# Kernel optimization log

Hardware: AMD Instinct MI355X
Metric: run time of the kernel (lower is better)

## Reference

```python
import jax, jax.numpy as jnp
import numpy as np
from jax import lax

B, T, S = 32, 64, 400
H, E, EMB, V = 512, 1024, 256, 32000


def setup_inputs() -> dict:
    key = jax.random.key(0)
    ks = jax.random.split(key, 16)
    w = lambda k, shape: jax.random.normal(k, shape, dtype=jnp.float32) * 0.05
    return {
        "target": jax.random.randint(ks[0], (B, T), 0, V),
        "h0": jax.random.normal(ks[1], (B, H), dtype=jnp.float32),
        "c0": jax.random.normal(ks[2], (B, H), dtype=jnp.float32),
        "enc_outs": jax.random.normal(ks[3], (S, B, E), dtype=jnp.float32),
        "attn_mask": jnp.ones((B, S), dtype=jnp.int32),
        "emb": w(ks[4], (V, EMB)),
        "W_ih": w(ks[5], (4 * H, EMB)),
        "b_ih": w(ks[6], (4 * H,)),
        "W_hh": w(ks[7], (4 * H, H)),
        "b_hh": w(ks[8], (4 * H,)),
        "W_attn": w(ks[9], (H, E)),
        "b_attn": w(ks[10], (H,)),
        "W_concat": w(ks[11], (H, E + H)),
        "b_concat": w(ks[12], (H,)),
        "W_out": w(ks[13], (V, H)),
        "b_out": w(ks[14], (V,)),
    }


def reference(target, h0, c0, enc_outs, attn_mask, emb, W_ih, b_ih, W_hh, b_hh,
              W_attn, b_attn, W_concat, b_concat, W_out, b_out):
    # Precompute attention keys projection once: [S, B, H]
    keys_proj = jnp.einsum("sbe,he->sbh", enc_outs, W_attn) + b_attn
    masked = attn_mask == 0  # [B, S]
    x_seq = emb[target].transpose(1, 0, 2)  # [T, B, EMB]

    def step(carry, x_t):
        h, c = carry
        # LSTMCell (torch gate order: i, f, g, o)
        gates = x_t @ W_ih.T + b_ih + h @ W_hh.T + b_hh  # [B, 4H]
        i, f, g, o = jnp.split(gates, 4, axis=1)
        c = jax.nn.sigmoid(f) * c + jax.nn.sigmoid(i) * jnp.tanh(g)
        h = jax.nn.sigmoid(o) * jnp.tanh(c)
        # additive-style attention: sum over hidden of query*key_proj
        scores = jnp.einsum("bh,sbh->bs", h, keys_proj)  # [B, S]
        scores = jnp.where(masked, jnp.float32(-1e18), scores)
        a = jax.nn.softmax(scores, axis=1)
        ctx = jnp.einsum("bs,sbe->be", a, enc_outs)  # [B, E]
        cat = jnp.tanh(jnp.concatenate([ctx, h], axis=1) @ W_concat.T + b_concat)
        logit = jax.nn.log_softmax(cat @ W_out.T + b_out, axis=-1)  # [B, V]
        return (h, c), logit

    (_, _), logits = lax.scan(step, (h0, c0), x_seq)  # [T, B, V]
    return logits.transpose(1, 0, 2)  # [B, T, V]
```

## Files before the change

kernel.cpp:

```cpp
#include <hip/hip_runtime.h>
#include <hip/hip_bf16.h>
#include <hip/hip_fp16.h>

#define B_ 32
#define T_ 64
#define S_ 400
#define SPAD_ 512
#define H_ 512
#define E_ 1024
#define EMB_ 256
#define V_ 32000
#define NCB_ 500

#define KEYS_BLOCKS 200
#define CVT_BLOCKS 48
#define MEGA_BLOCKS (8 + KEYS_BLOCKS + CVT_BLOCKS)
#define MEGA_LDS (65536 + 33280 + 4096 + 32)

typedef _Float16 f16;
typedef _Float16 half8 __attribute__((ext_vector_type(8)));
typedef float f32x4 __attribute__((ext_vector_type(4)));
typedef float f32x16 __attribute__((ext_vector_type(16)));
typedef unsigned uint4v __attribute__((ext_vector_type(4)));

__device__ __forceinline__ void gl_lds16(const void* g, void* l) {
  __builtin_amdgcn_global_load_lds(
      (const __attribute__((address_space(1))) void*)g,
      (__attribute__((address_space(3))) void*)l, 16, 0, 0);
}

__device__ __forceinline__ float sigmoidf_(float x) { return 1.f / (1.f + expf(-x)); }

__device__ __forceinline__ uint4v load_b128_sys(const void* p) {
  uint4v r;
  asm volatile("global_load_dwordx4 %0, %1, off sc0 sc1" : "=v"(r) : "v"(p) : "memory");
  return r;
}
__device__ __forceinline__ void store_b128_sys(void* p, uint4v v) {
  asm volatile("global_store_dwordx4 %0, %1, off sc0 sc1" :: "v"(p), "v"(v) : "memory");
}

__global__ __launch_bounds__(256) void gather_x_kernel(const int* __restrict__ target,
                                                       const float* __restrict__ emb,
                                                       f16* __restrict__ xin) {
  int r = blockIdx.x;
  int t = r >> 5, b = r & 31;
  int tok = target[b * T_ + t];
  xin[(size_t)r * EMB_ + threadIdx.x] = (f16)emb[(size_t)tok * EMB_ + threadIdx.x];
}

__global__ __launch_bounds__(256) void prep_kernel(const float* __restrict__ b_ih,
                                                   const float* __restrict__ b_hh,
                                                   float* __restrict__ biasperm,
                                                   const float* __restrict__ Whh,
                                                   f16* __restrict__ Wperm,
                                                   const float* __restrict__ Wih,
                                                   f16* __restrict__ Wihp,
                                                   const float* __restrict__ h0,
                                                   f16* __restrict__ hbuf,
                                                   const float* __restrict__ Wattn,
                                                   f16* __restrict__ Wattn_f) {
  int idx = blockIdx.x * 256 + threadIdx.x;
  if (idx < 4 * H_) {
    int j = idx >> 2, gg = idx & 3;
    biasperm[idx] = b_ih[gg * H_ + j] + b_hh[gg * H_ + j];
  }
  if (idx < B_ * H_) hbuf[idx] = (f16)h0[idx];
  if (idx < T_ * B_ * H_ / 8) {
    uint4v p = {0xFFFFFFFFu, 0xFFFFFFFFu, 0xFFFFFFFFu, 0xFFFFFFFFu};
    reinterpret_cast<uint4v*>(reinterpret_cast<char*>(hbuf) + (size_t)B_ * H_ * 2)[idx] = p;
  }
  {
    int j = idx >> 9, k = idx & 511;
#pragma unroll
    for (int gg = 0; gg < 4; ++gg)
      Wperm[((size_t)(j * 4 + gg)) * H_ + k] = (f16)Whh[((size_t)(gg * H_ + j)) * H_ + k];
  }
  if (idx < H_ * EMB_) {
    int j = idx >> 8, k = idx & 255;
#pragma unroll
    for (int gg = 0; gg < 4; ++gg)
      Wihp[((size_t)(j * 4 + gg)) * EMB_ + k] = (f16)Wih[((size_t)(gg * H_ + j)) * EMB_ + k];
  }
  {
    float2 v = reinterpret_cast<const float2*>(Wattn)[idx];
    union { f16 h[2]; unsigned u; } o;
    o.h[0] = (f16)v.x; o.h[1] = (f16)v.y;
    reinterpret_cast<unsigned*>(Wattn_f)[idx] = o.u;
  }
}

template <int OUTK, bool DO_TANH>
__global__ __launch_bounds__(256) void gemm_bt_kernel(const f16* __restrict__ A,
                                                      const f16* __restrict__ W,
                                                      const float* __restrict__ bias,
                                                      void* __restrict__ outp,
                                                      int M, int N, int K) {
  __shared__ __align__(16) char As[128 * 64];
  __shared__ __align__(16) char Bs[128 * 64];
  const int tid = threadIdx.x;
  const int lane = tid & 63, wave = tid >> 6;
  const int wr = (wave >> 1) * 64, wc = (wave & 1) * 64;
  const int fr = lane & 15, fq = lane >> 4;
  const int row0 = blockIdx.x * 128, col0 = blockIdx.y * 128;

  f32x4 acc[4][4];
#pragma unroll
  for (int i = 0; i < 4; ++i)
#pragma unroll
    for (int j = 0; j < 4; ++j) acc[i][j] = {0.f, 0.f, 0.f, 0.f};

  for (int k0 = 0; k0 < K; k0 += 32) {
    __syncthreads();
#pragma unroll
    for (int i = 0; i < 2; ++i) {
      int o = tid * 16 + i * 4096;
      int r = o >> 6, kk = (o & 63) >> 1;
      gl_lds16(A + (size_t)(row0 + r) * K + (k0 + kk), As + o);
      gl_lds16(W + (size_t)(col0 + r) * K + (k0 + kk), Bs + o);
    }
    __syncthreads();
    half8 af[4], bfr[4];
#pragma unroll
    for (int mi = 0; mi < 4; ++mi)
      af[mi] = *reinterpret_cast<const half8*>(As + (wr + mi * 16 + fr) * 64 + fq * 16);
#pragma unroll
    for (int ni = 0; ni < 4; ++ni)
      bfr[ni] = *reinterpret_cast<const half8*>(Bs + (wc + ni * 16 + fr) * 64 + fq * 16);
#pragma unroll
    for (int mi = 0; mi < 4; ++mi)
#pragma unroll
      for (int ni = 0; ni < 4; ++ni)
        acc[mi][ni] = __builtin_amdgcn_mfma_f32_16x16x32_f16(af[mi], bfr[ni], acc[mi][ni], 0, 0, 0);
  }

#pragma unroll
  for (int mi = 0; mi < 4; ++mi)
#pragma unroll
    for (int ni = 0; ni < 4; ++ni)
#pragma unroll
      for (int r = 0; r < 4; ++r) {
        int row = row0 + wr + mi * 16 + fq * 4 + r;
        int col = col0 + wc + ni * 16 + fr;
        float v = acc[mi][ni][r] + bias[col];
        if (DO_TANH) v = tanhf(v);
        if (OUTK == 0) {
          ((float*)outp)[(size_t)row * N + col] = v;
        } else if (OUTK == 1) {
          ((f16*)outp)[(size_t)row * N + col] = (f16)v;
        } else {
          int orow = (row & 31) * T_ + (row >> 5);
          ((float*)outp)[(size_t)orow * N + col] = v;
        }
      }
}

__global__ __launch_bounds__(512, 1) void mega_kernel(
    const float* __restrict__ xpart, const f16* __restrict__ Wperm,
    const float* __restrict__ c0, f16* __restrict__ hbuf,
    const float* __restrict__ enc, const f16* __restrict__ Wattn_f,
    const float* __restrict__ b_attn, f16* __restrict__ keys,
    const float* __restrict__ wc_src, f16* __restrict__ wc_dst,
    const float* __restrict__ wo_src, f16* __restrict__ wo_dst) {
  extern __shared__ char lds[];
  const int blk = blockIdx.x, tid = threadIdx.x;
  const int lane = tid & 63, wave = tid >> 6;

  if (blk < 8) {
    char* Abuf = lds;
    float* gates = (float*)(lds + 65536);
    unsigned* hstage = (unsigned*)(lds + 65536 + 33280);
    int* flags = (int*)(lds + 65536 + 33280 + 4096);
    const int g = blk;
    const int ln31 = lane & 31, lh = lane >> 5;

    if (tid < 8) flags[tid] = 0;

    half8 wf[32];
    {
      const f16* wrow = Wperm + ((size_t)(g * 256 + wave * 32 + ln31)) * H_ + lh * 8;
#pragma unroll
      for (int kc = 0; kc < 32; ++kc)
        wf[kc] = *reinterpret_cast<const half8*>(wrow + kc * 16);
    }

    const int b = tid >> 4, qd = tid & 15;
    float cst[4];
#pragma unroll
    for (int jj = 0; jj < 4; ++jj)
      cst[jj] = c0[b * H_ + g * 64 + qd * 4 + jj];

    __syncthreads();

    for (int t = 0; t < T_; ++t) {
      const float* xr = xpart + ((size_t)(t * B_ + b)) * (4 * H_) + g * 256 + qd * 16;
      float4 xv[4];
#pragma unroll
      for (int i = 0; i < 4; ++i) xv[i] = *reinterpret_cast<const float4*>(xr + i * 4);

      {
        int p = (t == 0) ? wave : (wave + (wave >= g ? 1 : 0));
        bool duty = (t == 0) ? true : (wave < 7);
        if (duty) {
          const char* sb = (const char*)hbuf + (size_t)t * 32768 + ln31 * 1024 + p * 128 + lh * 16;
          while (true) {
            uint4v v0 = load_b128_sys(sb);
            uint4v v1 = load_b128_sys(sb + 32);
            uint4v v2 = load_b128_sys(sb + 64);
            uint4v v3 = load_b128_sys(sb + 96);
            asm volatile("s_waitcnt vmcnt(0)" ::: "memory");
            __builtin_amdgcn_sched_barrier(0);
            unsigned bad = 0;
#pragma unroll
            for (int d = 0; d < 4; ++d)
              bad |= (unsigned)(v0[d] == 0xFFFFFFFFu) | (unsigned)(v1[d] == 0xFFFFFFFFu) |
                     (unsigned)(v2[d] == 0xFFFFFFFFu) | (unsigned)(v3[d] == 0xFFFFFFFFu);
            if (__all(bad == 0)) {
              char* ab = Abuf + (size_t)(t & 1) * 32768 + lane * 16;
              *(uint4v*)(ab + (size_t)(4 * p + 0) * 1024) = v0;
              *(uint4v*)(ab + (size_t)(4 * p + 1) * 1024) = v1;
              *(uint4v*)(ab + (size_t)(4 * p + 2) * 1024) = v2;
              *(uint4v*)(ab + (size_t)(4 * p + 3) * 1024) = v3;
              asm volatile("s_waitcnt lgkmcnt(0)" ::: "memory");
              __builtin_amdgcn_sched_barrier(0);
              if (lane == 0)
                __hip_atomic_fetch_add(&flags[p], 1, __ATOMIC_RELAXED,
                                       __HIP_MEMORY_SCOPE_WORKGROUP);
              break;
            }
          }
        }
      }

      f32x16 acc;
#pragma unroll
      for (int r = 0; r < 16; ++r) acc[r] = 0.f;
      const char* abR = Abuf + (size_t)(t & 1) * 32768 + lane * 16;
      const char* hsR = (const char*)hstage + lane * 16;
      const int thr = t + 1;
#pragma unroll
      for (int ps = 0; ps < 8; ++ps) {
        if (ps == g && t > 0) {
#pragma unroll
          for (int c = 0; c < 4; ++c) {
            half8 a = *(const half8*)(hsR + c * 1024);
            acc = __builtin_amdgcn_mfma_f32_32x32x16_f16(a, wf[4 * ps + c], acc, 0, 0, 0);
          }
        } else {
          while (__hip_atomic_load(&flags[ps], __ATOMIC_ACQUIRE,
                                   __HIP_MEMORY_SCOPE_WORKGROUP) < thr) {}
#pragma unroll
          for (int c = 0; c < 4; ++c) {
            half8 a = *(const half8*)(abR + (size_t)(4 * ps + c) * 1024);
            acc = __builtin_amdgcn_mfma_f32_32x32x16_f16(a, wf[4 * ps + c], acc, 0, 0, 0);
          }
        }
      }
      const int ln31b = lane & 31, lhb = lane >> 5;
#pragma unroll
      for (int r = 0; r < 16; ++r) {
        int row = (r & 3) + 8 * (r >> 2) + 4 * lhb;
        gates[row * 260 + wave * 32 + ln31b] = acc[r];
      }
      __syncthreads();

      const float* gr = &gates[b * 260 + qd * 16];
      float hv[4];
#pragma unroll
      for (int jj = 0; jj < 4; ++jj) {
        float gi = gr[jj * 4 + 0] + xv[jj].x;
        float gf = gr[jj * 4 + 1] + xv[jj].y;
        float gg = gr[jj * 4 + 2] + xv[jj].z;
        float go = gr[jj * 4 + 3] + xv[jj].w;
        cst[jj] = sigmoidf_(gf) * cst[jj] + sigmoidf_(gi) * tanhf(gg);
        hv[jj] = sigmoidf_(go) * tanhf(cst[jj]);
      }
      union { f16 h[2]; unsigned u; } pk0, pk1;
      pk0.h[0] = (f16)hv[0]; pk0.h[1] = (f16)hv[1];
      pk1.h[0] = (f16)hv[2]; pk1.h[1] = (f16)hv[3];
      {
        int cp0 = 2 * qd, cp1 = 2 * qd + 1;
        hstage[((cp0 >> 3) * 64 + ((cp0 >> 2) & 1) * 32 + b) * 4 + (cp0 & 3)] = pk0.u;
        hstage[((cp1 >> 3) * 64 + ((cp1 >> 2) & 1) * 32 + b) * 4 + (cp1 & 3)] = pk1.u;
      }
      __syncthreads();

      if (tid < 256) {
        int kcl = tid >> 6, l2 = tid & 63;
        uint4v v = *(const uint4v*)((const char*)hstage + (kcl * 64 + l2) * 16);
        store_b128_sys((char*)hbuf + (size_t)(t + 1) * 32768 + (l2 & 31) * 1024 +
                           g * 128 + kcl * 32 + (l2 >> 5) * 16,
                       v);
      }
    }
  } else if (blk < 8 + KEYS_BLOCKS) {
    char* As = lds;
    char* Bs = lds + 16384;
    const int kid = blk - 8;
    const int row0 = (kid % 50) * 256, col0 = (kid / 50) * 128;
    const int wr = (wave >> 1) * 64, wc = (wave & 1) * 64;
    const int fr = lane & 15, fq = lane >> 4;

    f32x4 acc[4][4];
#pragma unroll
    for (int i = 0; i < 4; ++i)
#pragma unroll
      for (int j = 0; j < 4; ++j) acc[i][j] = {0.f, 0.f, 0.f, 0.f};

    for (int k0 = 0; k0 < E_; k0 += 32) {
      __syncthreads();
      float4 av[4];
#pragma unroll
      for (int i = 0; i < 4; ++i) {
        int idx = tid + i * 512;
        int r = idx >> 3, ck = (idx & 7) * 4;
        av[i] = *reinterpret_cast<const float4*>(enc + (size_t)(row0 + r) * E_ + k0 + ck);
      }
      {
        int o = tid * 16;
        int r = o >> 6, kk = (o & 63) >> 1;
        gl_lds16(Wattn_f + (size_t)(col0 + r) * E_ + (k0 + kk), Bs + o);
      }
#pragma unroll
      for (int i = 0; i < 4; ++i) {
        int idx = tid + i * 512;
        int r = idx >> 3, ck = (idx & 7) * 4;
        union { f16 h[4]; unsigned long long u; } p;
        p.h[0] = (f16)av[i].x; p.h[1] = (f16)av[i].y;
        p.h[2] = (f16)av[i].z; p.h[3] = (f16)av[i].w;
        *reinterpret_cast<unsigned long long*>(As + r * 64 + ck * 2) = p.u;
      }
      __syncthreads();
      half8 af[4], bf[4];
#pragma unroll
      for (int mi = 0; mi < 4; ++mi)
        af[mi] = *reinterpret_cast<const half8*>(As + (wr + mi * 16 + fr) * 64 + fq * 16);
#pragma unroll
      for (int ni = 0; ni < 4; ++ni)
        bf[ni] = *reinterpret_cast<const half8*>(Bs + (wc + ni * 16 + fr) * 64 + fq * 16);
#pragma unroll
      for (int mi = 0; mi < 4; ++mi)
#pragma unroll
        for (int ni = 0; ni < 4; ++ni)
          acc[mi][ni] = __builtin_amdgcn_mfma_f32_16x16x32_f16(af[mi], bf[ni], acc[mi][ni], 0, 0, 0);
    }
#pragma unroll
    for (int mi = 0; mi < 4; ++mi)
#pragma unroll
      for (int ni = 0; ni < 4; ++ni)
#pragma unroll
        for (int r = 0; r < 4; ++r) {
          int row = row0 + wr + mi * 16 + fq * 4 + r;
          int col = col0 + wc + ni * 16 + fr;
          keys[(size_t)row * H_ + col] = (f16)(acc[mi][ni][r] + b_attn[col]);
        }
  } else {
    const int N2WC = H_ * (E_ + H_) / 2, N2WO = V_ * H_ / 2;
    const int total = N2WC + N2WO;
    const int stride = CVT_BLOCKS * 512;
    for (int i = (blk - 8 - KEYS_BLOCKS) * 512 + tid; i < total; i += stride) {
      const float* s; f16* d; int j;
      if (i < N2WC) { s = wc_src; d = wc_dst; j = i; }
      else { s = wo_src; d = wo_dst; j = i - N2WC; }
      float2 v = reinterpret_cast<const float2*>(s)[j];
      union { f16 h[2]; unsigned u; } o;
      o.h[0] = (f16)v.x; o.h[1] = (f16)v.y;
      reinterpret_cast<unsigned*>(d)[j] = o.u;
    }
  }
}

__global__ __launch_bounds__(128) void catcopy_kernel(const f16* __restrict__ hseq,
                                                      f16* __restrict__ catin) {
  int r = blockIdx.x;
  const uint2* src = reinterpret_cast<const uint2*>(hseq + (size_t)r * H_);
  uint2* dst = reinterpret_cast<uint2*>(catin + (size_t)r * (E_ + H_) + E_);
  dst[threadIdx.x] = src[threadIdx.x];
}

__global__ __launch_bounds__(256) void scores_mfma_kernel(const f16* __restrict__ keys,
                                                          const f16* __restrict__ hseq,
                                                          float* __restrict__ attnw) {
  const int b = blockIdx.y;
  const int lane = threadIdx.x & 63, wave = threadIdx.x >> 6;
  const int ln31 = lane & 31, lh = lane >> 5;
  const int stile = blockIdx.x * 128 + wave * 32;
  const f16* ar  = keys + ((size_t)(stile + ln31) * B_ + b) * H_ + lh * 8;
  const f16* br0 = hseq + ((size_t)ln31 * B_ + b) * H_ + lh * 8;
  const f16* br1 = hseq + ((size_t)(ln31 + 32) * B_ + b) * H_ + lh * 8;
  f32x16 ac0, ac1;
#pragma unroll
  for (int r = 0; r < 16; ++r) { ac0[r] = 0.f; ac1[r] = 0.f; }
#pragma unroll
  for (int kc = 0; kc < 32; ++kc) {
    half8 a  = *reinterpret_cast<const half8*>(ar + kc * 16);
    half8 h0 = *reinterpret_cast<const half8*>(br0 + kc * 16);
    half8 h1 = *reinterpret_cast<const half8*>(br1 + kc * 16);
    ac0 = __builtin_amdgcn_mfma_f32_32x32x16_f16(a, h0, ac0, 0, 0, 0);
    ac1 = __builtin_amdgcn_mfma_f32_32x32x16_f16(a, h1, ac1, 0, 0, 0);
  }
#pragma unroll
  for (int r = 0; r < 16; ++r) {
    int s = stile + (r & 3) + 8 * (r >> 2) + 4 * lh;
    if (s < S_) {
      attnw[((size_t)b * S_ + s) * T_ + ln31]      = ac0[r];
      attnw[((size_t)b * S_ + s) * T_ + 32 + ln31] = ac1[r];
    }
  }
}

__global__ __launch_bounds__(64) void softmax_kernel(float* __restrict__ attnw,
                                                     const int* __restrict__ mask) {
  int b = blockIdx.x, t = blockIdx.y, l = threadIdx.x;
  float vals[7];
  float m = -3.4e38f;
#pragma unroll
  for (int i = 0; i < 7; ++i) {
    int s = l + i * 64;
    float v = -3.4e38f;
    if (s < S_) {
      v = attnw[((size_t)b * S_ + s) * T_ + t];
      if (mask[b * S_ + s] == 0) v = -1e18f;
    }
    vals[i] = v;
    m = fmaxf(m, v);
  }
#pragma unroll
  for (int o = 32; o > 0; o >>= 1) m = fmaxf(m, __shfl_xor(m, o));
  float sum = 0.f;
#pragma unroll
  for (int i = 0; i < 7; ++i) {
    int s = l + i * 64;
    if (s < S_) { float e = expf(vals[i] - m); vals[i] = e; sum += e; }
  }
#pragma unroll
  for (int o = 32; o > 0; o >>= 1) sum += __shfl_xor(sum, o);
  float inv = 1.f / sum;
#pragma unroll
  for (int i = 0; i < 7; ++i) {
    int s = l + i * 64;
    if (s < S_) attnw[((size_t)b * S_ + s) * T_ + t] = vals[i] * inv;
  }
}

__global__ __launch_bounds__(256) void ctx_kernel(const float* __restrict__ attnw,
                                                  const float* __restrict__ enc,
                                                  f16* __restrict__ catin) {
  int b = blockIdx.x, e0 = blockIdx.y * 64;
  int el = threadIdx.x & 63, tq = threadIdx.x >> 6;
  __shared__ float a_lds[100 * 64];
  float acc[16];
#pragma unroll
  for (int i = 0; i < 16; ++i) acc[i] = 0.f;
  for (int sc = 0; sc < 4; ++sc) {
    __syncthreads();
    for (int i = threadIdx.x; i < 6400; i += 256)
      a_lds[i] = attnw[((size_t)b * S_ + sc * 100) * T_ + i];
    __syncthreads();
    for (int sl = 0; sl < 100; ++sl) {
      int s = sc * 100 + sl;
      float v = enc[((size_t)s * B_ + b) * E_ + e0 + el];
#pragma unroll
      for (int i = 0; i < 16; ++i) acc[i] += a_lds[sl * 64 + tq * 16 + i] * v;
    }
  }
#pragma unroll
  for (int i = 0; i < 16; ++i) {
    int t = tq * 16 + i;
    catin[((size_t)t * B_ + b) * (E_ + H_) + e0 + el] = (f16)acc[i];
  }
}

__global__ __launch_bounds__(256) void gemm_out_kernel(const f16* __restrict__ A,
                                                       const f16* __restrict__ W,
                                                       const float* __restrict__ bias,
                                                       f16* __restrict__ lbuf,
                                                       float* __restrict__ pm,
                                                       float* __restrict__ ps) {
  __shared__ __align__(16) char As[128 * 64];
  __shared__ __align__(16) char Bs[128 * 64];
  const int tid = threadIdx.x;
  const int lane = tid & 63, wave = tid >> 6;
  const int wr = (wave >> 1) * 64, wc = (wave & 1) * 64;
  const int fr = lane & 15, fq = lane >> 4;
  const int row0 = blockIdx.x * 128, col0 = blockIdx.y * 128;

  f32x4 acc[4][4];
#pragma unroll
  for (int i = 0; i < 4; ++i)
#pragma unroll
    for (int j = 0; j < 4; ++j) acc[i][j] = {0.f, 0.f, 0.f, 0.f};

  for (int k0 = 0; k0 < H_; k0 += 32) {
    __syncthreads();
#pragma unroll
    for (int i = 0; i < 2; ++i) {
      int o = tid * 16 + i * 4096;
      int r = o >> 6, kk = (o & 63) >> 1;
      gl_lds16(A + (size_t)(row0 + r) * H_ + (k0 + kk), As + o);
      gl_lds16(W + (size_t)(col0 + r) * H_ + (k0 + kk), Bs + o);
    }
    __syncthreads();
    half8 af[4], bfr[4];
#pragma unroll
    for (int mi = 0; mi < 4; ++mi)
      af[mi] = *reinterpret_cast<const half8*>(As + (wr + mi * 16 + fr) * 64 + fq * 16);
#pragma unroll
    for (int ni = 0; ni < 4; ++ni)
      bfr[ni] = *reinterpret_cast<const half8*>(Bs + (wc + ni * 16 + fr) * 64 + fq * 16);
#pragma unroll
    for (int mi = 0; mi < 4; ++mi)
#pragma unroll
      for (int ni = 0; ni < 4; ++ni)
        acc[mi][ni] = __builtin_amdgcn_mfma_f32_16x16x32_f16(af[mi], bfr[ni], acc[mi][ni], 0, 0, 0);
  }

#pragma unroll
  for (int mi = 0; mi < 4; ++mi)
#pragma unroll
    for (int r = 0; r < 4; ++r) {
      int row = row0 + wr + mi * 16 + fq * 4 + r;
      float v0 = acc[mi][0][r] + bias[col0 + wc + fr];
      float v1 = acc[mi][1][r] + bias[col0 + wc + 16 + fr];
      float v2 = acc[mi][2][r] + bias[col0 + wc + 32 + fr];
      float v3 = acc[mi][3][r] + bias[col0 + wc + 48 + fr];
      f16* lp = lbuf + (size_t)row * V_ + col0 + wc + fr;
      lp[0] = (f16)v0; lp[16] = (f16)v1; lp[32] = (f16)v2; lp[48] = (f16)v3;
      float mx = fmaxf(fmaxf(v0, v1), fmaxf(v2, v3));
#pragma unroll
      for (int d2 = 1; d2 <= 8; d2 <<= 1) mx = fmaxf(mx, __shfl_xor(mx, d2));
      float sm = expf(v0 - mx) + expf(v1 - mx) + expf(v2 - mx) + expf(v3 - mx);
#pragma unroll
      for (int d2 = 1; d2 <= 8; d2 <<= 1) sm += __shfl_xor(sm, d2);
      if (fr == 0) {
        int cb = (col0 + wc) >> 6;
        pm[(size_t)row * NCB_ + cb] = mx;
        ps[(size_t)row * NCB_ + cb] = sm;
      }
    }
}

__global__ __launch_bounds__(64) void lse_combine_kernel(const float* __restrict__ pm,
                                                         const float* __restrict__ ps,
                                                         float* __restrict__ lse) {
  int row = blockIdx.x, l = threadIdx.x;
  float mv[8], sv[8];
  float m = -3.4e38f;
#pragma unroll
  for (int i = 0; i < 8; ++i) {
    int idx = l + i * 64;
    if (idx < NCB_) {
      mv[i] = pm[(size_t)row * NCB_ + idx];
      sv[i] = ps[(size_t)row * NCB_ + idx];
    } else { mv[i] = -3.4e38f; sv[i] = 0.f; }
    m = fmaxf(m, mv[i]);
  }
#pragma unroll
  for (int o = 32; o > 0; o >>= 1) m = fmaxf(m, __shfl_xor(m, o));
  float s = 0.f;
#pragma unroll
  for (int i = 0; i < 8; ++i) s += sv[i] * expf(mv[i] - m);
#pragma unroll
  for (int o = 32; o > 0; o >>= 1) s += __shfl_xor(s, o);
  if (l == 0) lse[row] = m + logf(s);
}

__global__ __launch_bounds__(256) void final_out_kernel(const f16* __restrict__ lbuf,
                                                        const float* __restrict__ lse,
                                                        float* __restrict__ out) {
  int j = blockIdx.x;
  int b = j >> 6, t = j & 63;
  int r = t * B_ + b;
  float l = lse[r];
  const half8* src = reinterpret_cast<const half8*>(lbuf + (size_t)r * V_);
  float4* dst = reinterpret_cast<float4*>(out + (size_t)j * V_);
  for (int c = threadIdx.x; c < V_ / 8; c += 256) {
    half8 h = src[c];
    float4 o1, o2;
    o1.x = (float)h[0] - l; o1.y = (float)h[1] - l;
    o1.z = (float)h[2] - l; o1.w = (float)h[3] - l;
    o2.x = (float)h[4] - l; o2.y = (float)h[5] - l;
    o2.z = (float)h[6] - l; o2.w = (float)h[7] - l;
    dst[c * 2] = o1; dst[c * 2 + 1] = o2;
  }
}

__global__ __launch_bounds__(512, 1) void logsm_kernel(float* __restrict__ out) {
  int r = blockIdx.x;
  size_t base = (size_t)r * V_;
  int tid = threadIdx.x;
  float4* op = reinterpret_cast<float4*>(out + base);
  float4 v[16];
  float m = -3.4e38f;
#pragma unroll
  for (int k = 0; k < 16; ++k) {
    int c = tid + (k << 9);
    if (c < 8000) {
      v[k] = op[c];
      m = fmaxf(m, fmaxf(fmaxf(v[k].x, v[k].y), fmaxf(v[k].z, v[k].w)));
    }
  }
  __shared__ float red[8];
#pragma unroll
  for (int o = 32; o > 0; o >>= 1) m = fmaxf(m, __shfl_xor(m, o));
  if ((tid & 63) == 0) red[tid >> 6] = m;
  __syncthreads();
  float mm = red[0];
#pragma unroll
  for (int i = 1; i < 8; ++i) mm = fmaxf(mm, red[i]);
  float s = 0.f;
#pragma unroll
  for (int k = 0; k < 16; ++k) {
    int c = tid + (k << 9);
    if (c < 8000)
      s += expf(v[k].x - mm) + expf(v[k].y - mm) + expf(v[k].z - mm) + expf(v[k].w - mm);
  }
#pragma unroll
  for (int o = 32; o > 0; o >>= 1) s += __shfl_xor(s, o);
  __syncthreads();
  if ((tid & 63) == 0) red[tid >> 6] = s;
  __syncthreads();
  s = 0.f;
#pragma unroll
  for (int i = 0; i < 8; ++i) s += red[i];
  float lse = mm + logf(s);
#pragma unroll
  for (int k = 0; k < 16; ++k) {
    int c = tid + (k << 9);
    if (c < 8000) {
      float4 o4;
      o4.x = v[k].x - lse; o4.y = v[k].y - lse;
      o4.z = v[k].z - lse; o4.w = v[k].w - lse;
      op[c] = o4;
    }
  }
}

extern "C" void kernel_launch(void* const* d_in, const int* in_sizes, int n_in,
                              void* d_out, int out_size, void* d_ws, size_t ws_size,
                              hipStream_t stream) {
  const int*   target = (const int*)d_in[0];
  const float* h0     = (const float*)d_in[1];
  const float* c0     = (const float*)d_in[2];
  const float* enc    = (const float*)d_in[3];
  const int*   mask   = (const int*)d_in[4];
  const float* emb    = (const float*)d_in[5];
  const float* W_ih   = (const float*)d_in[6];
  const float* b_ih   = (const float*)d_in[7];
  const float* W_hh   = (const float*)d_in[8];
  const float* b_hh   = (const float*)d_in[9];
  const float* W_attn = (const float*)d_in[10];
  const float* b_attn = (const float*)d_in[11];
  const float* W_cat  = (const float*)d_in[12];
  const float* b_cat  = (const float*)d_in[13];
  const float* W_out  = (const float*)d_in[14];
  const float* b_out  = (const float*)d_in[15];

  char* ws = (char*)d_ws;
  size_t off = 0;
  auto alloc = [&](size_t bytes) {
    void* p = ws + off;
    off = (off + bytes + 255) & ~(size_t)255;
    return p;
  };
  f16*   keys_f   = (f16*)alloc((size_t)SPAD_ * B_ * H_ * 2);
  f16*   Wattn_f  = (f16*)alloc((size_t)H_ * E_ * 2);
  f16*   Wcat_f   = (f16*)alloc((size_t)H_ * (E_ + H_) * 2);
  f16*   Wout_f   = (f16*)alloc((size_t)V_ * H_ * 2);
  f16*   Wperm    = (f16*)alloc((size_t)4 * H_ * H_ * 2);
  f16*   Wihp     = (f16*)alloc((size_t)4 * H_ * EMB_ * 2);
  float* biasperm = (float*)alloc((size_t)4 * H_ * 4);
  f16*   xin_f    = (f16*)alloc((size_t)T_ * B_ * EMB_ * 2);
  float* xpart    = (float*)alloc((size_t)T_ * B_ * 4 * H_ * 4);
  f16*   catin_f  = (f16*)alloc((size_t)T_ * B_ * (E_ + H_) * 2);
  float* attnw    = (float*)alloc((size_t)B_ * S_ * T_ * 4);
  f16*   catbuf_f = (f16*)alloc((size_t)T_ * B_ * H_ * 2);
  f16*   hbuf     = (f16*)alloc((size_t)(T_ + 1) * B_ * H_ * 2);

  size_t extra = ((size_t)T_ * B_ * V_ * 2 + 255 + (size_t)T_ * B_ * NCB_ * 4 * 2 + 512 +
                  (size_t)T_ * B_ * 4 + 256);
  bool pathA = (off + extra) <= ws_size;
  f16* lbuf = nullptr; float* pm = nullptr; float* psb = nullptr; float* lse = nullptr;
  if (pathA) {
    lbuf = (f16*)alloc((size_t)T_ * B_ * V_ * 2);
    pm   = (float*)alloc((size_t)T_ * B_ * NCB_ * 4);
    psb  = (float*)alloc((size_t)T_ * B_ * NCB_ * 4);
    lse  = (float*)alloc((size_t)T_ * B_ * 4);
  }
  (void)in_sizes; (void)n_in; (void)out_size;

  f16* hseq_f = hbuf + (size_t)B_ * H_;

  gather_x_kernel<<<T_ * B_, 256, 0, stream>>>(target, emb, xin_f);
  prep_kernel<<<(H_ * H_) / 256, 256, 0, stream>>>(b_ih, b_hh, biasperm, W_hh, Wperm,
                                                   W_ih, Wihp, h0, hbuf, W_attn, Wattn_f);
  gemm_bt_kernel<0, false><<<dim3((T_ * B_) / 128, (4 * H_) / 128), 256, 0, stream>>>(
      xin_f, Wihp, biasperm, xpart, T_ * B_, 4 * H_, EMB_);

  mega_kernel<<<MEGA_BLOCKS, 512, MEGA_LDS, stream>>>(
      xpart, Wperm, c0, hbuf, enc, Wattn_f, b_attn, keys_f,
      W_cat, Wcat_f, W_out, Wout_f);

  catcopy_kernel<<<T_ * B_, 128, 0, stream>>>(hseq_f, catin_f);
  scores_mfma_kernel<<<dim3(SPAD_ / 128, B_), 256, 0, stream>>>(keys_f, hseq_f, attnw);
  softmax_kernel<<<dim3(B_, T_), 64, 0, stream>>>(attnw, mask);
  ctx_kernel<<<dim3(B_, E_ / 64), 256, 0, stream>>>(attnw, enc, catin_f);

  gemm_bt_kernel<1, true><<<dim3((T_ * B_) / 128, H_ / 128), 256, 0, stream>>>(
      catin_f, Wcat_f, b_cat, catbuf_f, T_ * B_, H_, E_ + H_);

  if (pathA) {
    gemm_out_kernel<<<dim3((T_ * B_) / 128, V_ / 128), 256, 0, stream>>>(
        catbuf_f, Wout_f, b_out, lbuf, pm, psb);
    lse_combine_kernel<<<T_ * B_, 64, 0, stream>>>(pm, psb, lse);
    final_out_kernel<<<T_ * B_, 256, 0, stream>>>(lbuf, lse, (float*)d_out);
  } else {
    gemm_bt_kernel<2, false><<<dim3((T_ * B_) / 128, V_ / 128), 256, 0, stream>>>(
        catbuf_f, Wout_f, b_out, (float*)d_out, T_ * B_, V_, H_);
    logsm_kernel<<<B_ * T_, 512, 0, stream>>>((float*)d_out);
  }
}
```

Baseline: 745.2 us.

## Fuse input projection into recurrent megakernel and merge attention post-processing kernels

Moves the x@W_ih projection GEMM into the persistent mega kernel as extra blocks that write xpart with system-scope stores. The recurrent blocks poll xpart against a 0xFFFFFFFF sentinel that prep_kernel pre-fills. It also fuses scores and softmax into one per-batch kernel using LDS, folds the hseq catcopy into the ctx kernel, and widens the output GEMM tile to 256 rows with 512 threads. The goal is to remove several launches and overlap the projection with the recurrence, at the cost of spin-waiting and fewer blocks for the keys GEMM.

```diff
diff --git a/kernel.cpp b/kernel.cpp
--- a/kernel.cpp
+++ b/kernel.cpp
@@ -12,9 +12,10 @@
 #define V_ 32000
 #define NCB_ 500
 
-#define KEYS_BLOCKS 200
+#define XPART_BLOCKS 16
+#define KEYS_BLOCKS 184
 #define CVT_BLOCKS 48
-#define MEGA_BLOCKS (8 + KEYS_BLOCKS + CVT_BLOCKS)
+#define MEGA_BLOCKS (8 + XPART_BLOCKS + KEYS_BLOCKS + CVT_BLOCKS)
 #define MEGA_LDS (65536 + 33280 + 4096 + 32)
 
 typedef _Float16 f16;
@@ -38,6 +39,9 @@
 }
 __device__ __forceinline__ void store_b128_sys(void* p, uint4v v) {
   asm volatile("global_store_dwordx4 %0, %1, off sc0 sc1" :: "v"(p), "v"(v) : "memory");
+}
+__device__ __forceinline__ void store_b32_sys(void* p, unsigned v) {
+  asm volatile("global_store_dword %0, %1, off sc0 sc1" :: "v"(p), "v"(v) : "memory");
 }
 
 __global__ __launch_bounds__(256) void gather_x_kernel(const int* __restrict__ target,
@@ -59,17 +63,21 @@
                                                    const float* __restrict__ h0,
                                                    f16* __restrict__ hbuf,
                                                    const float* __restrict__ Wattn,
-                                                   f16* __restrict__ Wattn_f) {
+                                                   f16* __restrict__ Wattn_f,
+                                                   float* __restrict__ xpart) {
   int idx = blockIdx.x * 256 + threadIdx.x;
   if (idx < 4 * H_) {
     int j = idx >> 2, gg = idx & 3;
     biasperm[idx] = b_ih[gg * H_ + j] + b_hh[gg * H_ + j];
   }
   if (idx < B_ * H_) hbuf[idx] = (f16)h0[idx];
+  uint4v p = {0xFFFFFFFFu, 0xFFFFFFFFu, 0xFFFFFFFFu, 0xFFFFFFFFu};
   if (idx < T_ * B_ * H_ / 8) {
-    uint4v p = {0xFFFFFFFFu, 0xFFFFFFFFu, 0xFFFFFFFFu, 0xFFFFFFFFu};
     reinterpret_cast<uint4v*>(reinterpret_cast<char*>(hbuf) + (size_t)B_ * H_ * 2)[idx] = p;
   }
+#pragma unroll
+  for (int i = 0; i < 4; ++i)
+    reinterpret_cast<uint4v*>(xpart)[idx + i * 262144] = p;
   {
     int j = idx >> 9, k = idx & 511;
 #pragma unroll
@@ -156,8 +164,10 @@
 }
 
 __global__ __launch_bounds__(512, 1) void mega_kernel(
-    const float* __restrict__ xpart, const f16* __restrict__ Wperm,
-    const float* __restrict__ c0, f16* __restrict__ hbuf,
+    const f16* __restrict__ xin, const f16* __restrict__ Wihp,
+    const float* __restrict__ biasperm, float* __restrict__ xpart,
+    const f16* __restrict__ Wperm, const float* __restrict__ c0,
+    f16* __restrict__ hbuf,
     const float* __restrict__ enc, const f16* __restrict__ Wattn_f,
     const float* __restrict__ b_attn, f16* __restrict__ keys,
     const float* __restrict__ wc_src, f16* __restrict__ wc_dst,
@@ -194,9 +204,9 @@
 
     for (int t = 0; t < T_; ++t) {
       const float* xr = xpart + ((size_t)(t * B_ + b)) * (4 * H_) + g * 256 + qd * 16;
-      float4 xv[4];
-#pragma unroll
-      for (int i = 0; i < 4; ++i) xv[i] = *reinterpret_cast<const float4*>(xr + i * 4);
+      uint4v xw[4];
+#pragma unroll
+      for (int i = 0; i < 4; ++i) xw[i] = load_b128_sys(xr + i * 4);
 
       {
         int p = (t == 0) ? wave : (wave + (wave >= g ? 1 : 0));
@@ -232,6 +242,30 @@
         }
       }
 
+      asm volatile("s_waitcnt vmcnt(0)" ::: "memory");
+      __builtin_amdgcn_sched_barrier(0);
+      unsigned xbad = 0;
+#pragma unroll
+      for (int i = 0; i < 4; ++i)
+#pragma unroll
+        for (int d = 0; d < 4; ++d) xbad |= (unsigned)(xw[i][d] == 0xFFFFFFFFu);
+      while (__any(xbad != 0)) {
+#pragma unroll
+        for (int i = 0; i < 4; ++i) xw[i] = load_b128_sys(xr + i * 4);
+        asm volatile("s_waitcnt vmcnt(0)" ::: "memory");
+        __builtin_amdgcn_sched_barrier(0);
+        xbad = 0;
+#pragma unroll
+        for (int i = 0; i < 4; ++i)
+#pragma unroll
+          for (int d = 0; d < 4; ++d) xbad |= (unsigned)(xw[i][d] == 0xFFFFFFFFu);
+      }
+      float4 xv[4];
+#pragma unroll
+      for (int i = 0; i < 4; ++i) {
+        union { uint4v u; float4 f; } cv; cv.u = xw[i]; xv[i] = cv.f;
+      }
+
       f32x16 acc;
 #pragma unroll
       for (int r = 0; r < 16; ++r) acc[r] = 0.f;
@@ -256,11 +290,10 @@
           }
         }
       }
-      const int ln31b = lane & 31, lhb = lane >> 5;
 #pragma unroll
       for (int r = 0; r < 16; ++r) {
-        int row = (r & 3) + 8 * (r >> 2) + 4 * lhb;
-        gates[row * 260 + wave * 32 + ln31b] = acc[r];
+        int row = (r & 3) + 8 * (r >> 2) + 4 * lh;
+        gates[row * 260 + wave * 32 + ln31] = acc[r];
       }
       __syncthreads();
 
@@ -293,72 +326,121 @@
                        v);
       }
     }
-  } else if (blk < 8 + KEYS_BLOCKS) {
+  } else if (blk < 8 + XPART_BLOCKS) {
+    char* As = lds;
+    char* Bs = lds + 8192;
+    const int col0 = (blk - 8) * 128;
+    const int wr = (wave & 3) * 32, wc = (wave >> 2) * 64;
+    const int fr = lane & 15, fq = lane >> 4;
+    for (int rt = 0; rt < 16; ++rt) {
+      const int row0 = rt * 128;
+      f32x4 acc[2][4];
+#pragma unroll
+      for (int i = 0; i < 2; ++i)
+#pragma unroll
+        for (int j = 0; j < 4; ++j) acc[i][j] = {0.f, 0.f, 0.f, 0.f};
+      for (int k0 = 0; k0 < EMB_; k0 += 32) {
+        __syncthreads();
+        {
+          int o = tid * 16;
+          int r = o >> 6, kk = (o & 63) >> 1;
+          gl_lds16(xin + (size_t)(row0 + r) * EMB_ + (k0 + kk), As + o);
+          gl_lds16(Wihp + (size_t)(col0 + r) * EMB_ + (k0 + kk), Bs + o);
+        }
+        __syncthreads();
+        half8 af[2], bf[4];
+#pragma unroll
+        for (int mi = 0; mi < 2; ++mi)
+          af[mi] = *reinterpret_cast<const half8*>(As + (wr + mi * 16 + fr) * 64 + fq * 16);
+#pragma unroll
+        for (int ni = 0; ni < 4; ++ni)
+          bf[ni] = *reinterpret_cast<const half8*>(Bs + (wc + ni * 16 + fr) * 64 + fq * 16);
+#pragma unroll
+        for (int mi = 0; mi < 2; ++mi)
+#pragma unroll
+          for (int ni = 0; ni < 4; ++ni)
+            acc[mi][ni] = __builtin_amdgcn_mfma_f32_16x16x32_f16(af[mi], bf[ni], acc[mi][ni], 0, 0, 0);
+      }
+#pragma unroll
+      for (int mi = 0; mi < 2; ++mi)
+#pragma unroll
+        for (int ni = 0; ni < 4; ++ni)
+#pragma unroll
+          for (int r = 0; r < 4; ++r) {
+            int row = row0 + wr + mi * 16 + fq * 4 + r;
+            int col = col0 + wc + ni * 16 + fr;
+            union { float f; unsigned u; } cv;
+            cv.f = acc[mi][ni][r] + biasperm[col];
+            store_b32_sys((char*)xpart + ((size_t)row * 2048 + col) * 4, cv.u);
+          }
+    }
+  } else if (blk < 8 + XPART_BLOCKS + KEYS_BLOCKS) {
     char* As = lds;
     char* Bs = lds + 16384;
-    const int kid = blk - 8;
-    const int row0 = (kid % 50) * 256, col0 = (kid / 50) * 128;
     const int wr = (wave >> 1) * 64, wc = (wave & 1) * 64;
     const int fr = lane & 15, fq = lane >> 4;
-
-    f32x4 acc[4][4];
-#pragma unroll
-    for (int i = 0; i < 4; ++i)
-#pragma unroll
-      for (int j = 0; j < 4; ++j) acc[i][j] = {0.f, 0.f, 0.f, 0.f};
-
-    for (int k0 = 0; k0 < E_; k0 += 32) {
+    for (int kid = blk - 8 - XPART_BLOCKS; kid < 200; kid += KEYS_BLOCKS) {
+      const int row0 = (kid % 50) * 256, col0 = (kid / 50) * 128;
+      f32x4 acc[4][4];
+#pragma unroll
+      for (int i = 0; i < 4; ++i)
+#pragma unroll
+        for (int j = 0; j < 4; ++j) acc[i][j] = {0.f, 0.f, 0.f, 0.f};
+
+      for (int k0 = 0; k0 < E_; k0 += 32) {
+        __syncthreads();
+        float4 av[4];
+#pragma unroll
+        for (int i = 0; i < 4; ++i) {
+          int idx = tid + i * 512;
+          int r = idx >> 3, ck = (idx & 7) * 4;
+          av[i] = *reinterpret_cast<const float4*>(enc + (size_t)(row0 + r) * E_ + k0 + ck);
+        }
+        {
+          int o = tid * 16;
+          int r = o >> 6, kk = (o & 63) >> 1;
+          gl_lds16(Wattn_f + (size_t)(col0 + r) * E_ + (k0 + kk), Bs + o);
+        }
+#pragma unroll
+        for (int i = 0; i < 4; ++i) {
+          int idx = tid + i * 512;
+          int r = idx >> 3, ck = (idx & 7) * 4;
+          union { f16 h[4]; unsigned long long u; } p;
+          p.h[0] = (f16)av[i].x; p.h[1] = (f16)av[i].y;
+          p.h[2] = (f16)av[i].z; p.h[3] = (f16)av[i].w;
+          *reinterpret_cast<unsigned long long*>(As + r * 64 + ck * 2) = p.u;
+        }
+        __syncthreads();
+        half8 af[4], bf[4];
+#pragma unroll
+        for (int mi = 0; mi < 4; ++mi)
+          af[mi] = *reinterpret_cast<const half8*>(As + (wr + mi * 16 + fr) * 64 + fq * 16);
+#pragma unroll
+        for (int ni = 0; ni < 4; ++ni)
+          bf[ni] = *reinterpret_cast<const half8*>(Bs + (wc + ni * 16 + fr) * 64 + fq * 16);
+#pragma unroll
+        for (int mi = 0; mi < 4; ++mi)
+#pragma unroll
+          for (int ni = 0; ni < 4; ++ni)
+            acc[mi][ni] = __builtin_amdgcn_mfma_f32_16x16x32_f16(af[mi], bf[ni], acc[mi][ni], 0, 0, 0);
+      }
+#pragma unroll
+      for (int mi = 0; mi < 4; ++mi)
+#pragma unroll
+        for (int ni = 0; ni < 4; ++ni)
+#pragma unroll
+          for (int r = 0; r < 4; ++r) {
+            int row = row0 + wr + mi * 16 + fq * 4 + r;
+            int col = col0 + wc + ni * 16 + fr;
+            keys[(size_t)row * H_ + col] = (f16)(acc[mi][ni][r] + b_attn[col]);
+          }
       __syncthreads();
-      float4 av[4];
-#pragma unroll
-      for (int i = 0; i < 4; ++i) {
-        int idx = tid + i * 512;
-        int r = idx >> 3, ck = (idx & 7) * 4;
-        av[i] = *reinterpret_cast<const float4*>(enc + (size_t)(row0 + r) * E_ + k0 + ck);
-      }
-      {
-        int o = tid * 16;
-        int r = o >> 6, kk = (o & 63) >> 1;
-        gl_lds16(Wattn_f + (size_t)(col0 + r) * E_ + (k0 + kk), Bs + o);
-      }
-#pragma unroll
-      for (int i = 0; i < 4; ++i) {
-        int idx = tid + i * 512;
-        int r = idx >> 3, ck = (idx & 7) * 4;
-        union { f16 h[4]; unsigned long long u; } p;
-        p.h[0] = (f16)av[i].x; p.h[1] = (f16)av[i].y;
-        p.h[2] = (f16)av[i].z; p.h[3] = (f16)av[i].w;
-        *reinterpret_cast<unsigned long long*>(As + r * 64 + ck * 2) = p.u;
-      }
-      __syncthreads();
-      half8 af[4], bf[4];
-#pragma unroll
-      for (int mi = 0; mi < 4; ++mi)
-        af[mi] = *reinterpret_cast<const half8*>(As + (wr + mi * 16 + fr) * 64 + fq * 16);
-#pragma unroll
-      for (int ni = 0; ni < 4; ++ni)
-        bf[ni] = *reinterpret_cast<const half8*>(Bs + (wc + ni * 16 + fr) * 64 + fq * 16);
-#pragma unroll
-      for (int mi = 0; mi < 4; ++mi)
-#pragma unroll
-        for (int ni = 0; ni < 4; ++ni)
-          acc[mi][ni] = __builtin_amdgcn_mfma_f32_16x16x32_f16(af[mi], bf[ni], acc[mi][ni], 0, 0, 0);
-    }
-#pragma unroll
-    for (int mi = 0; mi < 4; ++mi)
-#pragma unroll
-      for (int ni = 0; ni < 4; ++ni)
-#pragma unroll
-        for (int r = 0; r < 4; ++r) {
-          int row = row0 + wr + mi * 16 + fq * 4 + r;
-          int col = col0 + wc + ni * 16 + fr;
-          keys[(size_t)row * H_ + col] = (f16)(acc[mi][ni][r] + b_attn[col]);
-        }
+    }
   } else {
     const int N2WC = H_ * (E_ + H_) / 2, N2WO = V_ * H_ / 2;
     const int total = N2WC + N2WO;
     const int stride = CVT_BLOCKS * 512;
-    for (int i = (blk - 8 - KEYS_BLOCKS) * 512 + tid; i < total; i += stride) {
+    for (int i = (blk - 8 - XPART_BLOCKS - KEYS_BLOCKS) * 512 + tid; i < total; i += stride) {
       const float* s; f16* d; int j;
       if (i < N2WC) { s = wc_src; d = wc_dst; j = i; }
       else { s = wo_src; d = wo_dst; j = i - N2WC; }
@@ -370,95 +452,102 @@
   }
 }
 
-__global__ __launch_bounds__(128) void catcopy_kernel(const f16* __restrict__ hseq,
-                                                      f16* __restrict__ catin) {
-  int r = blockIdx.x;
-  const uint2* src = reinterpret_cast<const uint2*>(hseq + (size_t)r * H_);
-  uint2* dst = reinterpret_cast<uint2*>(catin + (size_t)r * (E_ + H_) + E_);
-  dst[threadIdx.x] = src[threadIdx.x];
-}
-
-__global__ __launch_bounds__(256) void scores_mfma_kernel(const f16* __restrict__ keys,
-                                                          const f16* __restrict__ hseq,
-                                                          float* __restrict__ attnw) {
-  const int b = blockIdx.y;
-  const int lane = threadIdx.x & 63, wave = threadIdx.x >> 6;
+__global__ __launch_bounds__(512, 1) void scores_softmax_kernel(const f16* __restrict__ keys,
+                                                                const f16* __restrict__ hseq,
+                                                                const int* __restrict__ mask,
+                                                                float* __restrict__ attnw) {
+  __shared__ float sc[S_ * 64];
+  __shared__ float pr[2][8][64];
+  const int b = blockIdx.x;
+  const int tid = threadIdx.x;
+  const int lane = tid & 63, wave = tid >> 6;
   const int ln31 = lane & 31, lh = lane >> 5;
-  const int stile = blockIdx.x * 128 + wave * 32;
-  const f16* ar  = keys + ((size_t)(stile + ln31) * B_ + b) * H_ + lh * 8;
+
+  const f16* ar0 = keys + ((size_t)(wave * 64 + ln31) * B_ + b) * H_ + lh * 8;
+  const f16* ar1 = keys + ((size_t)(wave * 64 + 32 + ln31) * B_ + b) * H_ + lh * 8;
   const f16* br0 = hseq + ((size_t)ln31 * B_ + b) * H_ + lh * 8;
   const f16* br1 = hseq + ((size_t)(ln31 + 32) * B_ + b) * H_ + lh * 8;
-  f32x16 ac0, ac1;
-#pragma unroll
-  for (int r = 0; r < 16; ++r) { ac0[r] = 0.f; ac1[r] = 0.f; }
+  f32x16 a00, a01, a10, a11;
+#pragma unroll
+  for (int r = 0; r < 16; ++r) { a00[r] = 0.f; a01[r] = 0.f; a10[r] = 0.f; a11[r] = 0.f; }
 #pragma unroll
   for (int kc = 0; kc < 32; ++kc) {
-    half8 a  = *reinterpret_cast<const half8*>(ar + kc * 16);
+    half8 k0 = *reinterpret_cast<const half8*>(ar0 + kc * 16);
+    half8 k1 = *reinterpret_cast<const half8*>(ar1 + kc * 16);
     half8 h0 = *reinterpret_cast<const half8*>(br0 + kc * 16);
     half8 h1 = *reinterpret_cast<const half8*>(br1 + kc * 16);
-    ac0 = __builtin_amdgcn_mfma_f32_32x32x16_f16(a, h0, ac0, 0, 0, 0);
-    ac1 = __builtin_amdgcn_mfma_f32_32x32x16_f16(a, h1, ac1, 0, 0, 0);
+    a00 = __builtin_amdgcn_mfma_f32_32x32x16_f16(k0, h0, a00, 0, 0, 0);
+    a01 = __builtin_amdgcn_mfma_f32_32x32x16_f16(k0, h1, a01, 0, 0, 0);
+    a10 = __builtin_amdgcn_mfma_f32_32x32x16_f16(k1, h0, a10, 0, 0, 0);
+    a11 = __builtin_amdgcn_mfma_f32_32x32x16_f16(k1, h1, a11, 0, 0, 0);
   }
 #pragma unroll
   for (int r = 0; r < 16; ++r) {
-    int s = stile + (r & 3) + 8 * (r >> 2) + 4 * lh;
-    if (s < S_) {
-      attnw[((size_t)b * S_ + s) * T_ + ln31]      = ac0[r];
-      attnw[((size_t)b * S_ + s) * T_ + 32 + ln31] = ac1[r];
-    }
-  }
-}
-
-__global__ __launch_bounds__(64) void softmax_kernel(float* __restrict__ attnw,
-                                                     const int* __restrict__ mask) {
-  int b = blockIdx.x, t = blockIdx.y, l = threadIdx.x;
-  float vals[7];
+    int srow = (r & 3) + 8 * (r >> 2) + 4 * lh;
+    int s0 = wave * 64 + srow, s1 = wave * 64 + 32 + srow;
+    if (s0 < S_) { sc[s0 * 64 + ln31] = a00[r]; sc[s0 * 64 + 32 + ln31] = a01[r]; }
+    if (s1 < S_) { sc[s1 * 64 + ln31] = a10[r]; sc[s1 * 64 + 32 + ln31] = a11[r]; }
+  }
+  __syncthreads();
+
+  const int t = lane, si = wave;
   float m = -3.4e38f;
-#pragma unroll
-  for (int i = 0; i < 7; ++i) {
-    int s = l + i * 64;
-    float v = -3.4e38f;
-    if (s < S_) {
-      v = attnw[((size_t)b * S_ + s) * T_ + t];
-      if (mask[b * S_ + s] == 0) v = -1e18f;
-    }
-    vals[i] = v;
+  for (int i = 0; i < 50; ++i) {
+    int s = si * 50 + i;
+    float v = (mask[b * S_ + s] == 0) ? -1e18f : sc[s * 64 + t];
+    sc[s * 64 + t] = v;
     m = fmaxf(m, v);
   }
-#pragma unroll
-  for (int o = 32; o > 0; o >>= 1) m = fmaxf(m, __shfl_xor(m, o));
+  pr[0][si][t] = m;
+  __syncthreads();
+  float mt = pr[0][0][t];
+#pragma unroll
+  for (int j = 1; j < 8; ++j) mt = fmaxf(mt, pr[0][j][t]);
   float sum = 0.f;
-#pragma unroll
-  for (int i = 0; i < 7; ++i) {
-    int s = l + i * 64;
-    if (s < S_) { float e = expf(vals[i] - m); vals[i] = e; sum += e; }
-  }
-#pragma unroll
-  for (int o = 32; o > 0; o >>= 1) sum += __shfl_xor(sum, o);
-  float inv = 1.f / sum;
-#pragma unroll
-  for (int i = 0; i < 7; ++i) {
-    int s = l + i * 64;
-    if (s < S_) attnw[((size_t)b * S_ + s) * T_ + t] = vals[i] * inv;
-  }
-}
-
-__global__ __launch_bounds__(256) void ctx_kernel(const float* __restrict__ attnw,
-                                                  const float* __restrict__ enc,
-                                                  f16* __restrict__ catin) {
-  int b = blockIdx.x, e0 = blockIdx.y * 64;
+  for (int i = 0; i < 50; ++i) {
+    int s = si * 50 + i;
+    float e = expf(sc[s * 64 + t] - mt);
+    sc[s * 64 + t] = e;
+    sum += e;
+  }
+  pr[1][si][t] = sum;
+  __syncthreads();
+  float den = 0.f;
+#pragma unroll
+  for (int j = 0; j < 8; ++j) den += pr[1][j][t];
+  float inv = 1.f / den;
+  for (int i = 0; i < 50; ++i) {
+    int s = si * 50 + i;
+    attnw[((size_t)b * S_ + s) * T_ + t] = sc[s * 64 + t] * inv;
+  }
+}
+
+__global__ __launch_bounds__(256) void ctx_cat_kernel(const float* __restrict__ attnw,
+                                                      const float* __restrict__ enc,
+                                                      const f16* __restrict__ hseq,
+                                                      f16* __restrict__ catin) {
+  int b = blockIdx.x, y = blockIdx.y;
+  if (y == 16) {
+    for (int i = threadIdx.x; i < 64 * 64; i += 256) {
+      int t = i >> 6, c = i & 63;
+      uint4v v = *(const uint4v*)((const char*)hseq + ((size_t)t * B_ + b) * 1024 + c * 16);
+      *(uint4v*)((char*)catin + ((size_t)t * B_ + b) * 3072 + 2048 + c * 16) = v;
+    }
+    return;
+  }
+  int e0 = y * 64;
   int el = threadIdx.x & 63, tq = threadIdx.x >> 6;
   __shared__ float a_lds[100 * 64];
   float acc[16];
 #pragma unroll
   for (int i = 0; i < 16; ++i) acc[i] = 0.f;
-  for (int sc = 0; sc < 4; ++sc) {
+  for (int scn = 0; scn < 4; ++scn) {
     __syncthreads();
     for (int i = threadIdx.x; i < 6400; i += 256)
-      a_lds[i] = attnw[((size_t)b * S_ + sc * 100) * T_ + i];
+      a_lds[i] = attnw[((size_t)b * S_ + scn * 100) * T_ + i];
     __syncthreads();
     for (int sl = 0; sl < 100; ++sl) {
-      int s = sc * 100 + sl;
+      int s = scn * 100 + sl;
       float v = enc[((size_t)s * B_ + b) * E_ + e0 + el];
 #pragma unroll
       for (int i = 0; i < 16; ++i) acc[i] += a_lds[sl * 64 + tq * 16 + i] * v;
@@ -471,19 +560,19 @@
   }
 }
 
-__global__ __launch_bounds__(256) void gemm_out_kernel(const f16* __restrict__ A,
-                                                       const f16* __restrict__ W,
-                                                       const float* __restrict__ bias,
-                                                       f16* __restrict__ lbuf,
-                                                       float* __restrict__ pm,
-                                                       float* __restrict__ ps) {
-  __shared__ __align__(16) char As[128 * 64];
+__global__ __launch_bounds__(512) void gemm_out256_kernel(const f16* __restrict__ A,
+                                                          const f16* __restrict__ W,
+                                                          const float* __restrict__ bias,
+                                                          f16* __restrict__ lbuf,
+                                                          float* __restrict__ pm,
+                                                          float* __restrict__ ps) {
+  __shared__ __align__(16) char As[256 * 64];
   __shared__ __align__(16) char Bs[128 * 64];
   const int tid = threadIdx.x;
   const int lane = tid & 63, wave = tid >> 6;
   const int wr = (wave >> 1) * 64, wc = (wave & 1) * 64;
   const int fr = lane & 15, fq = lane >> 4;
-  const int row0 = blockIdx.x * 128, col0 = blockIdx.y * 128;
+  const int row0 = blockIdx.x * 256, col0 = blockIdx.y * 128;
 
   f32x4 acc[4][4];
 #pragma unroll
@@ -493,12 +582,13 @@
 
   for (int k0 = 0; k0 < H_; k0 += 32) {
     __syncthreads();
-#pragma unroll
-    for (int i = 0; i < 2; ++i) {
-      int o = tid * 16 + i * 4096;
+    {
+      int o = tid * 16;
       int r = o >> 6, kk = (o & 63) >> 1;
       gl_lds16(A + (size_t)(row0 + r) * H_ + (k0 + kk), As + o);
       gl_lds16(W + (size_t)(col0 + r) * H_ + (k0 + kk), Bs + o);
+      o += 8192; r = o >> 6; kk = (o & 63) >> 1;
+      gl_lds16(A + (size_t)(row0 + r) * H_ + (k0 + kk), As + o);
     }
     __syncthreads();
     half8 af[4], bfr[4];
@@ -693,24 +783,21 @@
 
   gather_x_kernel<<<T_ * B_, 256, 0, stream>>>(target, emb, xin_f);
   prep_kernel<<<(H_ * H_) / 256, 256, 0, stream>>>(b_ih, b_hh, biasperm, W_hh, Wperm,
-                                                   W_ih, Wihp, h0, hbuf, W_attn, Wattn_f);
-  gemm_bt_kernel<0, false><<<dim3((T_ * B_) / 128, (4 * H_) / 128), 256, 0, stream>>>(
-      xin_f, Wihp, biasperm, xpart, T_ * B_, 4 * H_, EMB_);
+                                                   W_ih, Wihp, h0, hbuf, W_attn, Wattn_f,
+                                                   xpart);
 
   mega_kernel<<<MEGA_BLOCKS, 512, MEGA_LDS, stream>>>(
-      xpart, Wperm, c0, hbuf, enc, Wattn_f, b_attn, keys_f,
-      W_cat, Wcat_f, W_out, Wout_f);
-
-  catcopy_kernel<<<T_ * B_, 128, 0, stream>>>(hseq_f, catin_f);
-  scores_mfma_kernel<<<dim3(SPAD_ / 128, B_), 256, 0, stream>>>(keys_f, hseq_f, attnw);
-  softmax_kernel<<<dim3(B_, T_), 64, 0, stream>>>(attnw, mask);
-  ctx_kernel<<<dim3(B_, E_ / 64), 256, 0, stream>>>(attnw, enc, catin_f);
+      xin_f, Wihp, biasperm, xpart, Wperm, c0, hbuf,
+      enc, Wattn_f, b_attn, keys_f, W_cat, Wcat_f, W_out, Wout_f);
+
+  scores_softmax_kernel<<<B_, 512, 0, stream>>>(keys_f, hseq_f, mask, attnw);
+  ctx_cat_kernel<<<dim3(B_, 17), 256, 0, stream>>>(attnw, enc, hseq_f, catin_f);
 
   gemm_bt_kernel<1, true><<<dim3((T_ * B_) / 128, H_ / 128), 256, 0, stream>>>(
       catin_f, Wcat_f, b_cat, catbuf_f, T_ * B_, H_, E_ + H_);
 
   if (pathA) {
-    gemm_out_kernel<<<dim3((T_ * B_) / 128, V_ / 128), 256, 0, stream>>>(
+    gemm_out256_kernel<<<dim3((T_ * B_) / 256, V_ / 128), 512, 0, stream>>>(
         catbuf_f, Wout_f, b_out, lbuf, pm, psb);
     lse_combine_kernel<<<T_ * B_, 64, 0, stream>>>(pm, psb, lse);
     final_out_kernel<<<T_ * B_, 256, 0, stream>>>(lbuf, lse, (float*)d_out);
```

Result: slower. 794.5 us (+6.6%).
